# Performance work log

Hardware: AMD Instinct MI355X
Metric: run time of the kernel (lower is better)

## Reference

```python
import jax, jax.numpy as jnp
import numpy as np

K = 16  # kNN neighbors (KnnEncoder default)


def _bn(h, g, s):
    # eval-mode BatchNorm with running mean 0 / var 1 folded into affine
    return h * g + s


def setup_inputs() -> dict:
    key = jax.random.key(0)
    cnt = [0]
    def nk():
        cnt[0] += 1
        return jax.random.fold_in(key, cnt[0])
    B, N = 4, 4096
    def W(i, o):
        return jax.random.normal(nk(), (i, o), jnp.float32) / np.float32(i) ** 0.5
    def bias(d):
        return jnp.zeros((d,), jnp.float32)
    def gamma(d):
        return jnp.ones((d,), jnp.float32) + 0.1 * jax.random.normal(nk(), (d,), jnp.float32)
    def beta(d):
        return 0.1 * jax.random.normal(nk(), (d,), jnp.float32)
    inp = dict(
        pos=jax.random.normal(nk(), (B, N, 3), jnp.float32),
        query_point_idx=jax.random.randint(nk(), (B,), 0, N),
        # PointNetConv local MLP: 6 -> 64 -> 128 -> 256 (plain last)
        cw1=W(6, 64), cb1=bias(64), cg1=gamma(64), cs1=beta(64),
        cw2=W(64, 128), cb2=bias(128), cg2=gamma(128), cs2=beta(128),
        cw3=W(128, 256), cb3=bias(256),
        # GlobalSAModule MLP: 259 -> 256 -> 512 -> 1024 (plain last)
        sw1=W(259, 256), sb1=bias(256), sg1=gamma(256), ss1=beta(256),
        sw2=W(256, 512), sb2=bias(512), sg2=gamma(512), ss2=beta(512),
        sw3=W(512, 1024), sb3=bias(1024),
        # EdgeGraspPredictor: 1280 -> 512 -> 256 -> 16
        pw1=W(1280, 512), pb1=bias(512),
        pw2=W(512, 256), pb2=bias(256),
        pw3=W(256, 16), pb3=bias(16),
    )
    return inp


def reference(pos, query_point_idx, cw1, cb1, cg1, cs1, cw2, cb2, cg2, cs2, cw3, cb3,
              sw1, sb1, sg1, ss1, sw2, sb2, sg2, ss2, sw3, sb3,
              pw1, pb1, pw2, pb2, pw3, pb3):
    B, N, _ = pos.shape
    # kNN within each cloud (self included, as torch_geometric knn with x==y)
    d2 = jnp.sum((pos[:, :, None, :] - pos[:, None, :, :]) ** 2, axis=-1)  # [B,N,N]
    _, idx = jax.lax.top_k(-d2, K)  # [B,N,K] targets for each source point n
    nbr = jax.vmap(lambda p, i: p[i])(pos, idx)  # [B,N,K,3] target positions
    # PointNetConv message: cat([x_j = pos_src, pos_src - pos_tgt])
    src = jnp.broadcast_to(pos[:, :, None, :], (B, N, K, 3))
    h = jnp.concatenate([src, src - nbr], axis=-1)  # [B,N,K,6]
    h = jnp.maximum(_bn(h @ cw1 + cb1, cg1, cs1), 0.0)
    h = jnp.maximum(_bn(h @ cw2 + cb2, cg2, cs2), 0.0)
    m = h @ cw3 + cb3  # [B,N,K,256] per-edge messages
    # scatter-max aggregation at target nodes (every node has its self edge)
    tgt = (idx + (jnp.arange(B) * N)[:, None, None]).reshape(-1)
    x = jax.ops.segment_max(m.reshape(-1, m.shape[-1]), tgt, num_segments=B * N)
    x = x.reshape(B, N, -1)  # [B,N,256] per-point features
    # GlobalSAModule: pointwise MLP then global max pool per cloud
    g = jnp.concatenate([x, pos], axis=-1)  # [B,N,259]
    g = jnp.maximum(_bn(g @ sw1 + sb1, sg1, ss1), 0.0)
    g = jnp.maximum(_bn(g @ sw2 + sb2, sg2, ss2), 0.0)
    g = g @ sw3 + sb3  # [B,N,1024]
    scene = jnp.max(g, axis=1)  # [B,1024]
    # gather query point feature, concat with scene feature, predictor MLP
    q = query_point_idx + jnp.arange(B) * N
    point_feat = x.reshape(B * N, -1)[q]  # [B,256]
    ef = jnp.concatenate([point_feat, scene], axis=-1)  # [B,1280]
    h = jnp.maximum(ef @ pw1 + pb1, 0.0)
    h = jnp.maximum(h @ pw2 + pb2, 0.0)
    return h @ pw3 + pb3  # [B,16]
```

## Files before the change

### kernel.cpp

```cpp
#include <hip/hip_runtime.h>

#define BB 4
#define NN 4096
#define KK 16

typedef unsigned short u16;
typedef unsigned int   u32;
typedef unsigned long long u64;

typedef __attribute__((ext_vector_type(8))) short bf16x8;
typedef __attribute__((ext_vector_type(4))) float f32x4;

__device__ __forceinline__ float b2f(u16 x){ return __uint_as_float(((u32)x) << 16); }
__device__ __forceinline__ u16 f2b(float f){
    u32 u = __float_as_uint(f);
    u32 r = (u + 0x7FFFu + ((u >> 16) & 1u)) >> 16;
    return (u16)r;
}
__device__ __forceinline__ u32 fmap(float f){
    u32 u = __float_as_uint(f);
    return (u & 0x80000000u) ? ~u : (u | 0x80000000u);
}
__device__ __forceinline__ float funmap(u32 u){
    u32 v = (u & 0x80000000u) ? (u ^ 0x80000000u) : ~u;
    return __uint_as_float(v);
}

#define N_ARR 27
__device__ const int ASZ[N_ARR] = {
    49152, 384, 64, 64, 64, 8192, 128, 128, 128, 32768, 256,
    66304, 256, 256, 256, 131072, 512, 512, 512, 524288, 1024,
    655360, 512, 131072, 256, 4096, 16 };
__device__ const int AOFF[N_ARR] = {
    0, 49152, 49536, 49600, 49664, 49728, 57920, 58048, 58176, 58304, 91072,
    91328, 157632, 157888, 158144, 158400, 289472, 289984, 290496, 291008, 815296,
    816320, 1471680, 1472192, 1603264, 1603520, 1607616 };

struct Ptrs { const void* p[N_ARR]; };

#define O_POS 0
#define O_CW1 49152
#define O_CB1 49536
#define O_CG1 49600
#define O_CS1 49664
#define O_CB2 57920
#define O_CG2 58048
#define O_CS2 58176
#define O_CB3 91072
#define O_SW1 91328
#define O_SB1 157632
#define O_SG1 157888
#define O_SS1 158144
#define O_SB2 289472
#define O_SG2 289984
#define O_SS2 290496
#define O_SB3 815296
#define O_PW1 816320
#define O_PB1 1471680
#define O_PW2 1472192
#define O_PB2 1603264
#define O_PW3 1603520
#define O_PB3 1607616

__global__ void detect_kernel(const u16* __restrict__ pos_u16, u32* __restrict__ flag){
    __shared__ int cnt;
    if (threadIdx.x == 0) cnt = 0;
    __syncthreads();
    int c = 0;
    #pragma unroll
    for (int s = 0; s < 4; ++s){
        u16 u = pos_u16[2*(threadIdx.x*4 + s)];
        int e = (u >> 7) & 0xFF;
        c += (e >= 0x68 && e <= 0x82) ? 1 : 0;
    }
    atomicAdd(&cnt, c);
    __syncthreads();
    if (threadIdx.x == 0) *flag = (cnt >= 512) ? 1u : 0u;
}

__device__ __forceinline__ void pack_one_src(const void* __restrict__ src, bool isbf,
                                             u16* __restrict__ dst, int tot, int log2n,
                                             int g, int T){
    const int nmask = (1 << log2n) - 1;
    for (int id = g; id < tot; id += T){
        int i = id & 7, lg = (id >> 3) & 3;
        int rest = id >> 5;
        int n = rest & nmask;
        int ks = rest >> log2n;
        int si = (ks*32 + lg*8 + i) << log2n | n;
        dst[id] = isbf ? ((const u16*)src)[si] : f2b(((const float*)src)[si]);
    }
}

__global__ __launch_bounds__(256) void prep_kernel(Ptrs pt, const u32* __restrict__ flagp,
        float* __restrict__ dst, float* __restrict__ psoa,
        u16* __restrict__ wp2, u16* __restrict__ wp3,
        u16* __restrict__ swp1, u16* __restrict__ swp2, u16* __restrict__ swp3){
    const bool isbf = (*flagp != 0);
    const int T = gridDim.x * 256;
    const int g = blockIdx.x * 256 + threadIdx.x;
    #pragma unroll
    for (int a = 0; a < N_ARR; ++a){
        if (a == 5 || a == 9 || a == 15 || a == 19) continue;
        const int sz = ASZ[a], off = AOFF[a];
        if (isbf){
            const u16* s = (const u16*)pt.p[a];
            for (int i = g; i < sz; i += T) dst[off + i] = b2f(s[i]);
        } else {
            const float* s = (const float*)pt.p[a];
            for (int i = g; i < sz; i += T) dst[off + i] = s[i];
        }
    }
    for (int i = g; i < BB*NN; i += T){
        float x, y, z;
        if (isbf){
            const u16* s = (const u16*)pt.p[0];
            x = b2f(s[3*i]); y = b2f(s[3*i+1]); z = b2f(s[3*i+2]);
        } else {
            const float* s = (const float*)pt.p[0];
            x = s[3*i]; y = s[3*i+1]; z = s[3*i+2];
        }
        psoa[i] = x; psoa[BB*NN + i] = y; psoa[2*BB*NN + i] = z;
    }
    pack_one_src(pt.p[5],  isbf, wp2,    8192,  7, g, T);
    pack_one_src(pt.p[9],  isbf, wp3,   32768,  8, g, T);
    pack_one_src(pt.p[11], isbf, swp1,  65536,  8, g, T);
    pack_one_src(pt.p[15], isbf, swp2, 131072,  9, g, T);
    pack_one_src(pt.p[19], isbf, swp3, 524288, 10, g, T);
}

__global__ __launch_bounds__(1024) void sort_kernel(const float* __restrict__ psoa,
        float* __restrict__ xs, float* __restrict__ ys, float* __restrict__ zs,
        int* __restrict__ sidx){
    __shared__ u64 s[NN];
    const int b = blockIdx.x;
    const int tid = threadIdx.x;
    const float* px = psoa + b*NN;
    const float* py = psoa + BB*NN + b*NN;
    const float* pz = psoa + 2*BB*NN + b*NN;
    for (int i = tid; i < NN; i += 1024)
        s[i] = (((u64)fmap(px[i])) << 32) | (u32)i;
    __syncthreads();
    for (int ksz = 2; ksz <= NN; ksz <<= 1){
        for (int jj = ksz >> 1; jj > 0; jj >>= 1){
            for (int t = tid; t < NN/2; t += 1024){
                int i  = ((t & ~(jj-1)) << 1) | (t & (jj-1));
                int ix = i | jj;
                u64 a = s[i], v = s[ix];
                bool up = ((i & ksz) == 0);
                if ((a > v) == up){ s[i] = v; s[ix] = a; }
            }
            __syncthreads();
        }
    }
    for (int r = tid; r < NN; r += 1024){
        u64 kv = s[r];
        int oi = (int)(u32)(kv & 0xFFFFFFFFu);
        xs[b*NN + r] = funmap((u32)(kv >> 32));
        ys[b*NN + r] = py[oi];
        zs[b*NN + r] = pz[oi];
        sidx[b*NN + r] = oi;
    }
}

#define QCAP 192
__device__ __forceinline__ void refine16(u64* __restrict__ buf, int& cnt, float& tau, int lane){
    u64 loc[3];
    #pragma unroll
    for (int q = 0; q < 3; ++q){
        int p = lane + (q << 6);
        loc[q] = (p < cnt) ? buf[p] : ~0ull;
    }
    u64 m = ~0ull;
    #pragma unroll
    for (int r = 0; r < KK; ++r){
        m = loc[0];
        m = loc[1] < m ? loc[1] : m;
        m = loc[2] < m ? loc[2] : m;
        #pragma unroll
        for (int off = 32; off > 0; off >>= 1){
            u64 o = __shfl_xor(m, off);
            m = o < m ? o : m;
        }
        if (lane == r) buf[r] = m;
        #pragma unroll
        for (int q = 0; q < 3; ++q) if (loc[q] == m) loc[q] = ~0ull;
    }
    cnt = KK;
    tau = __uint_as_float((u32)(m >> 32));
}

__global__ __launch_bounds__(512) void knn_kernel(
        const float* __restrict__ xs, const float* __restrict__ ys,
        const float* __restrict__ zs, const int* __restrict__ sidx,
        int* __restrict__ knn_out, u32* __restrict__ deg){
    __shared__ __align__(16) u64 kbuf[16*QCAP];
    const int b  = blockIdx.x >> 8;
    const int r0 = (blockIdx.x & 255) << 4;
    const float* X = xs + b*NN;
    const float* Y = ys + b*NN;
    const float* Z = zs + b*NN;
    const int*   S = sidx + b*NN;
    const int tid = threadIdx.x;
    const int lane = tid & 63;
    const int wv = tid >> 6;
    const int rA = r0 + wv*2, rB = rA + 1;
    const float axq = X[rA], ayq = Y[rA], azq = Z[rA];
    const float bxq = X[rB], byq = Y[rB], bzq = Z[rB];
    u64* bufA = kbuf + (wv*2)*QCAP;
    u64* bufB = bufA + QCAP;

    float tauA = 3.0e38f, tauB = 3.0e38f;
    int cntA = 0, cntB = 0;
    for (int k = 0; k < 128; ++k){
        int j = (lane < 32) ? (rA - 1 - (k << 5) - lane)
                            : (rA + (k << 5) + (lane - 32));
        bool inr = ((u32)j < (u32)NN);
        int ja = inr ? j : rA;
        float cx = X[ja], cy = Y[ja], cz = Z[ja];
        int sorig = S[ja];
        float dxA = axq - cx, dyA = ayq - cy, dzA = azq - cz;
        float d2A = __fadd_rn(__fadd_rn(__fmul_rn(dxA,dxA), __fmul_rn(dyA,dyA)), __fmul_rn(dzA,dzA));
        float dxB = bxq - cx, dyB = byq - cy, dzB = bzq - cz;
        float d2B = __fadd_rn(__fadd_rn(__fmul_rn(dxB,dxB), __fmul_rn(dyB,dyB)), __fmul_rn(dzB,dzB));
        bool pA = inr && (d2A <= tauA);
        u64 balA = __ballot(pA);
        if (balA){
            int nins = __popcll(balA);
            if (cntA + nins > QCAP) refine16(bufA, cntA, tauA, lane);
            if (pA){
                int ofs = __popcll(balA & ((1ull << lane) - 1ull));
                bufA[cntA + ofs] = (((u64)__float_as_uint(d2A)) << 32) | (u32)sorig;
            }
            cntA += nins;
        }
        bool pB = inr && (d2B <= tauB);
        u64 balB = __ballot(pB);
        if (balB){
            int nins = __popcll(balB);
            if (cntB + nins > QCAP) refine16(bufB, cntB, tauB, lane);
            if (pB){
                int ofs = __popcll(balB & ((1ull << lane) - 1ull));
                bufB[cntB + ofs] = (((u64)__float_as_uint(d2B)) << 32) | (u32)sorig;
            }
            cntB += nins;
        }
        int lo = rA - ((k + 1) << 5) - 1;
        int hi = rA + ((k + 1) << 5);
        float xlo = (lo >= 0) ? X[lo] : -3.0e38f;
        float xhi = (hi < NN) ? X[hi] :  3.0e38f;
        float dLa = axq - xlo, dRa = xhi - axq;
        float dLb = bxq - xlo, dRb = xhi - bxq;
        if (dLa*dLa > tauA && dRa*dRa > tauA && dLb*dLb > tauB && dRb*dRb > tauB) break;
    }
    refine16(bufA, cntA, tauA, lane);
    refine16(bufB, cntB, tauB, lane);
    const int origA = S[rA], origB = S[rB];
    if (lane < KK){
        u64 kA = bufA[lane];
        int jA = (int)(u32)(kA & 0xFFFFFFFFu);
        knn_out[((size_t)(b*NN + origA))*KK + lane] = jA;
        atomicAdd(deg + (b << 12) + jA, 1u);
        u64 kB = bufB[lane];
        int jB = (int)(u32)(kB & 0xFFFFFFFFu);
        knn_out[((size_t)(b*NN + origB))*KK + lane] = jB;
        atomicAdd(deg + (b << 12) + jB, 1u);
    }
}

__global__ __launch_bounds__(1024) void scan_kernel(const u32* __restrict__ deg,
                                                    int* __restrict__ rowstart, u32* __restrict__ cursor){
    __shared__ int lsum[1024];
    const int tid = threadIdx.x;
    const int base = tid * 16;
    int loc[16]; int s = 0;
    #pragma unroll
    for (int q = 0; q < 16; ++q){ loc[q] = (int)deg[base+q]; s += loc[q]; }
    lsum[tid] = s;
    __syncthreads();
    int acc = s;
    for (int ofs = 1; ofs < 1024; ofs <<= 1){
        int t = (tid >= ofs) ? lsum[tid-ofs] : 0;
        __syncthreads();
        acc += t; lsum[tid] = acc;
        __syncthreads();
    }
    int excl = acc - s;
    #pragma unroll
    for (int q = 0; q < 16; ++q){
        rowstart[base+q] = excl; cursor[base+q] = (u32)excl; excl += loc[q];
    }
    if (tid == 1023) rowstart[16384] = excl;
}

__global__ __launch_bounds__(256) void fill_kernel(const int* __restrict__ knn,
                                                   u32* __restrict__ cursor, int* __restrict__ csr){
    int e = blockIdx.x*256 + threadIdx.x;
    int b = e >> 16;
    int t = (b << 12) + knn[e];
    u32 pos = atomicAdd(cursor + t, 1u);
    csr[pos] = e;
}

__device__ __forceinline__ bf16x8 ldfrag(const u16* h, int row, int kofs, int rowstride){
    u32 byte = (u32)((row*rowstride + kofs)*2) ^ (u32)((row & 7) << 4);
    return *(const bf16x8*)((const char*)h + byte);
}
__device__ __forceinline__ void st16(u16* h, int row, int col, int rowstride, float v){
    u32 byte = (u32)((row*rowstride + col)*2) ^ (u32)((row & 7) << 4);
    *(u16*)((char*)h + byte) = f2b(v);
}

__global__ __launch_bounds__(256, 2) void edge_kernel(
    const float* __restrict__ conv, const int* __restrict__ knn,
    const int* __restrict__ rowstart, const int* __restrict__ csr,
    const u16* __restrict__ wp2, const u16* __restrict__ wp3,
    u16* __restrict__ xh)
{
    __shared__ float in6[6][64];
    __shared__ int   lts[64];
    __shared__ int   rs_l[17];
    __shared__ float scw1[384];
    __shared__ float sc1[64], sh1[64];
    __shared__ __align__(16) u16 h1s[64*64];
    __shared__ __align__(16) u16 h2s[64*128];
    __shared__ u32 lsx[16*256];

    const float* posf = conv + O_POS;
    const float* cb1 = conv + O_CB1; const float* cg1 = conv + O_CG1; const float* cs1 = conv + O_CS1;

    const int tid = threadIdx.x;
    const int w   = tid >> 6;
    const int l   = tid & 63;
    const int t0  = blockIdx.x << 4;
    const int b   = t0 >> 12;

    if (tid < 64){ float g1 = cg1[tid]; sc1[tid]=g1; sh1[tid]=cb1[tid]*g1 + cs1[tid]; }
    if (tid < 17) rs_l[tid] = rowstart[t0 + tid];
    for (int u = tid; u < 384; u += 256) scw1[u] = conv[O_CW1 + u];
    #pragma unroll
    for (int q = 0; q < 16; ++q) lsx[q*256 + tid] = 0u;

    const int lr = l & 15, lg = l >> 4;
    const int colb2 = w << 5;
    const int colb3 = w << 6;

    float sc2v[2], sh2v[2], bs3v[4];
    #pragma unroll
    for (int nt = 0; nt < 2; ++nt){
        int c = colb2 + nt*16 + lr;
        float g2 = conv[O_CG2 + c];
        sc2v[nt] = g2; sh2v[nt] = conv[O_CB2 + c]*g2 + conv[O_CS2 + c];
    }
    #pragma unroll
    for (int nt = 0; nt < 4; ++nt) bs3v[nt] = conv[O_CB3 + colb3 + nt*16 + lr];

    __syncthreads();
    const int segstart = rs_l[0], segend = rs_l[16];
    const int nchunk = (segend - segstart + 63) >> 6;

    int curl = -1;
    float run[4];
    #pragma unroll
    for (int nt = 0; nt < 4; ++nt) run[nt] = 0.f;

    for (int ch = 0; ch < nchunk; ++ch){
        __syncthreads();
        if (tid < 64){
            int gpos = segstart + (ch << 6) + tid;
            int lt = -1;
            float ax=0,ay=0,az=0,dx=0,dy=0,dz=0;
            if (gpos < segend){
                lt = 0;
                #pragma unroll
                for (int q = 1; q < 16; ++q) lt += (gpos >= rs_l[q]) ? 1 : 0;
                int e = csr[gpos];
                int i = (e >> 4) & (NN - 1);
                int j = knn[e];
                const float* pi = posf + ((size_t)(b*NN + i))*3;
                const float* pj = posf + ((size_t)(b*NN + j))*3;
                ax = pi[0]; ay = pi[1]; az = pi[2];
                dx = ax - pj[0]; dy = ay - pj[1]; dz = az - pj[2];
            }
            lts[tid] = lt;
            in6[0][tid]=ax; in6[1][tid]=ay; in6[2][tid]=az;
            in6[3][tid]=dx; in6[4][tid]=dy; in6[5][tid]=dz;
        }
        __syncthreads();

        {
            const int e = tid & 63, c0g = (tid >> 6) << 4;
            float a0=in6[0][e], a1=in6[1][e], a2=in6[2][e],
                  a3=in6[3][e], a4=in6[4][e], a5=in6[5][e];
            u32 pk[8];
            #pragma unroll
            for (int ci = 0; ci < 16; ++ci){
                int cc = c0g + ci;
                float acc = a0*scw1[cc]     + a1*scw1[64+cc]  + a2*scw1[128+cc]
                          + a3*scw1[192+cc] + a4*scw1[256+cc] + a5*scw1[320+cc];
                float v = fmaxf(acc*sc1[cc] + sh1[cc], 0.f);
                u32 h = (u32)f2b(v);
                if (ci & 1) pk[ci >> 1] |= h << 16; else pk[ci >> 1] = h;
            }
            u32 base = (u32)(e*128 + c0g*2);
            u32 swz  = (u32)((e & 7) << 4);
            *(uint4*)((char*)h1s + (base ^ swz))        = make_uint4(pk[0],pk[1],pk[2],pk[3]);
            *(uint4*)((char*)h1s + ((base + 16) ^ swz)) = make_uint4(pk[4],pk[5],pk[6],pk[7]);
        }
        __syncthreads();

        {
            f32x4 acc2[4][2];
            #pragma unroll
            for (int mt = 0; mt < 4; ++mt)
                #pragma unroll
                for (int nt = 0; nt < 2; ++nt) acc2[mt][nt] = (f32x4){0.f,0.f,0.f,0.f};
            #pragma unroll
            for (int ks = 0; ks < 2; ++ks){
                bf16x8 bf[2];
                #pragma unroll
                for (int nt = 0; nt < 2; ++nt)
                    bf[nt] = *(const bf16x8*)(wp2 + (((ks*128 + colb2 + nt*16 + lr) << 2) + lg)*8);
                #pragma unroll
                for (int mt = 0; mt < 4; ++mt){
                    bf16x8 a = ldfrag(h1s, mt*16 + lr, ks*32 + lg*8, 64);
                    #pragma unroll
                    for (int nt = 0; nt < 2; ++nt)
                        acc2[mt][nt] = __builtin_amdgcn_mfma_f32_16x16x32_bf16(a, bf[nt], acc2[mt][nt], 0, 0, 0);
                }
            }
            #pragma unroll
            for (int mt = 0; mt < 4; ++mt)
                #pragma unroll
                for (int nt = 0; nt < 2; ++nt)
                    #pragma unroll
                    for (int r = 0; r < 4; ++r){
                        int row = mt*16 + lg*4 + r;
                        float v = fmaxf(acc2[mt][nt][r]*sc2v[nt] + sh2v[nt], 0.f);
                        st16(h2s, row, colb2 + nt*16 + lr, 128, v);
                    }
        }
        __syncthreads();

        {
            f32x4 acc3[4][4];
            #pragma unroll
            for (int mt = 0; mt < 4; ++mt)
                #pragma unroll
                for (int nt = 0; nt < 4; ++nt) acc3[mt][nt] = (f32x4){0.f,0.f,0.f,0.f};
            #pragma unroll
            for (int ks = 0; ks < 4; ++ks){
                bf16x8 bf[4];
                #pragma unroll
                for (int nt = 0; nt < 4; ++nt)
                    bf[nt] = *(const bf16x8*)(wp3 + (((ks*256 + colb3 + nt*16 + lr) << 2) + lg)*8);
                #pragma unroll
                for (int mt = 0; mt < 4; ++mt){
                    bf16x8 a = ldfrag(h2s, mt*16 + lr, ks*32 + lg*8, 128);
                    #pragma unroll
                    for (int nt = 0; nt < 4; ++nt)
                        acc3[mt][nt] = __builtin_amdgcn_mfma_f32_16x16x32_bf16(a, bf[nt], acc3[mt][nt], 0, 0, 0);
                }
            }
            #pragma unroll
            for (int mt = 0; mt < 4; ++mt)
                #pragma unroll
                for (int r = 0; r < 4; ++r){
                    int row = mt*16 + lg*4 + r;
                    int lt = lts[row];
                    if (lt != curl){
                        if (curl >= 0){
                            #pragma unroll
                            for (int nt = 0; nt < 4; ++nt)
                                atomicMax(&lsx[curl*256 + colb3 + nt*16 + lr], fmap(run[nt]));
                        }
                        curl = lt;
                        #pragma unroll
                        for (int nt = 0; nt < 4; ++nt) run[nt] = acc3[mt][nt][r] + bs3v[nt];
                    } else {
                        #pragma unroll
                        for (int nt = 0; nt < 4; ++nt) run[nt] = fmaxf(run[nt], acc3[mt][nt][r] + bs3v[nt]);
                    }
                }
        }
    }
    if (curl >= 0){
        #pragma unroll
        for (int nt = 0; nt < 4; ++nt)
            atomicMax(&lsx[curl*256 + colb3 + nt*16 + lr], fmap(run[nt]));
    }
    __syncthreads();
    #pragma unroll
    for (int q = 0; q < 16; ++q)
        xh[((size_t)(t0+q))*256 + tid] = f2b(funmap(lsx[q*256 + tid]));
}

__global__ __launch_bounds__(256, 3) void sa_kernel(
    const float* __restrict__ conv, const u16* __restrict__ xh,
    const u16* __restrict__ swp1, const u16* __restrict__ swp2, const u16* __restrict__ swp3,
    u32* __restrict__ scene_map)
{
    __shared__ __align__(16) u16 h1s[32*256];
    __shared__ __align__(16) u16 h2s[32*512];
    __shared__ float spw[3][256];
    __shared__ float spx[32], spy[32], spz[32];

    const int tid = threadIdx.x;
    const int w   = tid >> 6;
    const int l   = tid & 63;
    const int lr  = l & 15, lg = l >> 4;
    const int b   = blockIdx.x >> 7;
    const int n0  = (blockIdx.x & 127) << 5;
    const u16* xrow = xh + ((size_t)(b*NN + n0))*256;

    if (tid < 96){
        int p = tid & 31, d = tid >> 5;
        float v = conv[O_POS + ((size_t)(b*NN + n0 + p))*3 + d];
        if (d == 0) spx[p] = v; else if (d == 1) spy[p] = v; else spz[p] = v;
    }
    for (int u = tid; u < 768; u += 256)
        spw[u >> 8][u & 255] = conv[O_SW1 + (256 + (u >> 8))*256 + (u & 255)];
    __syncthreads();

    {
        const int c0 = w << 6;
        float sc1v[4], sh1v[4];
        #pragma unroll
        for (int nt = 0; nt < 4; ++nt){
            int cc = c0 + nt*16 + lr;
            float g = conv[O_SG1 + cc];
            sc1v[nt] = g; sh1v[nt] = conv[O_SB1 + cc]*g + conv[O_SS1 + cc];
        }
        f32x4 acc[2][4];
        #pragma unroll
        for (int mt = 0; mt < 2; ++mt)
            #pragma unroll
            for (int nt = 0; nt < 4; ++nt)
                #pragma unroll
                for (int r = 0; r < 4; ++r){
                    int row = mt*16 + lg*4 + r;
                    int cc  = c0 + nt*16 + lr;
                    acc[mt][nt][r] = spx[row]*spw[0][cc] + spy[row]*spw[1][cc] + spz[row]*spw[2][cc];
                }
        #pragma unroll
        for (int ks = 0; ks < 8; ++ks){
            bf16x8 bf[4];
            #pragma unroll
            for (int nt = 0; nt < 4; ++nt)
                bf[nt] = *(const bf16x8*)(swp1 + (((ks*256 + c0 + nt*16 + lr) << 2) + lg)*8);
            #pragma unroll
            for (int mt = 0; mt < 2; ++mt){
                bf16x8 a = *(const bf16x8*)(xrow + (mt*16 + lr)*256 + ks*32 + lg*8);
                #pragma unroll
                for (int nt = 0; nt < 4; ++nt)
                    acc[mt][nt] = __builtin_amdgcn_mfma_f32_16x16x32_bf16(a, bf[nt], acc[mt][nt], 0, 0, 0);
            }
        }
        #pragma unroll
        for (int mt = 0; mt < 2; ++mt)
            #pragma unroll
            for (int nt = 0; nt < 4; ++nt)
                #pragma unroll
                for (int r = 0; r < 4; ++r){
                    int row = mt*16 + lg*4 + r;
                    float v = fmaxf(acc[mt][nt][r]*sc1v[nt] + sh1v[nt], 0.f);
                    st16(h1s, row, c0 + nt*16 + lr, 256, v);
                }
    }
    __syncthreads();

    {
        const int c0 = w << 7;
        float sc2v[8], sh2v[8];
        #pragma unroll
        for (int nt = 0; nt < 8; ++nt){
            int cc = c0 + nt*16 + lr;
            float g = conv[O_SG2 + cc];
            sc2v[nt] = g; sh2v[nt] = conv[O_SB2 + cc]*g + conv[O_SS2 + cc];
        }
        f32x4 acc[2][8];
        #pragma unroll
        for (int mt = 0; mt < 2; ++mt)
            #pragma unroll
            for (int nt = 0; nt < 8; ++nt) acc[mt][nt] = (f32x4){0.f,0.f,0.f,0.f};
        #pragma unroll
        for (int ks = 0; ks < 8; ++ks){
            bf16x8 bf[8];
            #pragma unroll
            for (int nt = 0; nt < 8; ++nt)
                bf[nt] = *(const bf16x8*)(swp2 + (((ks*512 + c0 + nt*16 + lr) << 2) + lg)*8);
            #pragma unroll
            for (int mt = 0; mt < 2; ++mt){
                bf16x8 a = ldfrag(h1s, mt*16 + lr, ks*32 + lg*8, 256);
                #pragma unroll
                for (int nt = 0; nt < 8; ++nt)
                    acc[mt][nt] = __builtin_amdgcn_mfma_f32_16x16x32_bf16(a, bf[nt], acc[mt][nt], 0, 0, 0);
            }
        }
        #pragma unroll
        for (int mt = 0; mt < 2; ++mt)
            #pragma unroll
            for (int nt = 0; nt < 8; ++nt)
                #pragma unroll
                for (int r = 0; r < 4; ++r){
                    int row = mt*16 + lg*4 + r;
                    float v = fmaxf(acc[mt][nt][r]*sc2v[nt] + sh2v[nt], 0.f);
                    st16(h2s, row, c0 + nt*16 + lr, 512, v);
                }
    }
    __syncthreads();

    #pragma unroll
    for (int half = 0; half < 2; ++half){
        const int c0 = (half << 9) + (w << 7);
        f32x4 acc[2][8];
        #pragma unroll
        for (int mt = 0; mt < 2; ++mt)
            #pragma unroll
            for (int nt = 0; nt < 8; ++nt) acc[mt][nt] = (f32x4){0.f,0.f,0.f,0.f};
        #pragma unroll
        for (int ks = 0; ks < 16; ++ks){
            bf16x8 bf[8];
            #pragma unroll
            for (int nt = 0; nt < 8; ++nt)
                bf[nt] = *(const bf16x8*)(swp3 + (((ks*1024 + c0 + nt*16 + lr) << 2) + lg)*8);
            #pragma unroll
            for (int mt = 0; mt < 2; ++mt){
                bf16x8 a = ldfrag(h2s, mt*16 + lr, ks*32 + lg*8, 512);
                #pragma unroll
                for (int nt = 0; nt < 8; ++nt)
                    acc[mt][nt] = __builtin_amdgcn_mfma_f32_16x16x32_bf16(a, bf[nt], acc[mt][nt], 0, 0, 0);
            }
        }
        #pragma unroll
        for (int nt = 0; nt < 8; ++nt){
            float v = acc[0][nt][0];
            #pragma unroll
            for (int mt = 0; mt < 2; ++mt)
                #pragma unroll
                for (int r = 0; r < 4; ++r) v = fmaxf(v, acc[mt][nt][r]);
            v = fmaxf(v, __shfl_xor(v, 16));
            v = fmaxf(v, __shfl_xor(v, 32));
            if (lg == 0){
                int cc = c0 + nt*16 + lr;
                atomicMax(scene_map + (b << 10) + cc, fmap(v + conv[O_SB3 + cc]));
            }
        }
    }
}

__global__ __launch_bounds__(128) void head1_kernel(
    const float* __restrict__ conv,
    const u16* __restrict__ xh, const u32* __restrict__ scene_map, const int* __restrict__ qidx,
    float* __restrict__ h1out)
{
    __shared__ float ef[1280];
    __shared__ float psum[4][32];
    const float* pw1 = conv + O_PW1; const float* pb1 = conv + O_PB1;
    const int b  = blockIdx.x >> 4;
    const int c0 = (blockIdx.x & 15) << 5;
    const int tid = threadIdx.x;
    const int q = qidx[b];
    for (int u = tid; u < 1280; u += 128){
        float v;
        if (u < 256) v = b2f(xh[(((size_t)(b*NN + q)) << 8) + u]);
        else         v = funmap(scene_map[(b << 10) + (u - 256)]);
        ef[u] = v;
    }
    __syncthreads();
    const int c = c0 + (tid & 31);
    const int rc = tid >> 5;
    float acc = 0.f;
    for (int r = rc*320; r < rc*320 + 320; ++r) acc += ef[r] * pw1[r*512 + c];
    psum[rc][tid & 31] = acc;
    __syncthreads();
    if (tid < 32){
        float a = psum[0][tid] + psum[1][tid] + psum[2][tid] + psum[3][tid] + pb1[c0 + tid];
        h1out[(b << 9) + c0 + tid] = fmaxf(a, 0.f);
    }
}

__global__ __launch_bounds__(256) void head2_kernel(
    const float* __restrict__ conv, const float* __restrict__ h1in,
    const u32* __restrict__ flagp, void* __restrict__ outv)
{
    __shared__ float h1[4][512];
    __shared__ float h2[4][256];
    const float* pw2 = conv + O_PW2; const float* pb2 = conv + O_PB2;
    const float* pw3 = conv + O_PW3; const float* pb3 = conv + O_PB3;
    const int tid = threadIdx.x;
    for (int u = tid; u < 2048; u += 256) h1[u >> 9][u & 511] = h1in[u];
    __syncthreads();
    for (int o = tid; o < 1024; o += 256){
        int b = o >> 8, c = o & 255;
        float acc = pb2[c];
        for (int r = 0; r < 512; ++r) acc += h1[b][r] * pw2[r*256 + c];
        h2[b][c] = fmaxf(acc, 0.f);
    }
    __syncthreads();
    if (tid < 64){
        int b = tid >> 4, c = tid & 15;
        float acc = pb3[c];
        for (int r = 0; r < 256; ++r) acc += h2[b][r] * pw3[r*16 + c];
        if (*flagp) ((u16*)outv)[tid] = f2b(acc);
        else        ((float*)outv)[tid] = acc;
    }
}

extern "C" void kernel_launch(void* const* d_in, const int* in_sizes, int n_in,
                              void* d_out, int out_size, void* d_ws, size_t ws_size,
                              hipStream_t stream){
    (void)in_sizes; (void)n_in; (void)out_size; (void)ws_size;
    const int* qidx = (const int*)d_in[1];

    char* ws = (char*)d_ws;
    u32*  flag      = (u32*)ws;
    float* conv     = (float*)(ws + 1024);
    u16*  wp2       = (u16*)(ws + 6432768);
    u16*  wp3       = (u16*)(ws + 6449152);
    u16*  swp1      = (u16*)(ws + 6514688);
    u16*  swp2      = (u16*)(ws + 6645760);
    u16*  swp3      = (u16*)(ws + 6907904);
    int*  knn       = (int*)(ws + 7956480);
    u32*  deg       = (u32*)(ws + 9005056);
    u32*  scene_map = (u32*)(ws + 9070592);
    int*  rowstart  = (int*)(ws + 9086976);
    u32*  cursor    = (u32*)(ws + 9152576);
    int*  csr       = (int*)(ws + 9218112);
    u16*  xh        = (u16*)(ws + 10266688);
    float* h1ws     = (float*)(ws + 18655296);
    float* psoa     = (float*)(ws + 18663488);
    float* xs       = (float*)(ws + 18860096);
    float* ys       = (float*)(ws + 18925632);
    float* zs       = (float*)(ws + 18991168);
    int*   sidx     = (int*)(ws + 19056704);

    Ptrs pt;
    pt.p[0] = d_in[0];
    for (int k = 1; k < N_ARR; ++k) pt.p[k] = d_in[k + 1];

    hipMemsetAsync(ws + 9005056, 0, 81920, stream);

    detect_kernel <<<1, 256, 0, stream>>>((const u16*)d_in[0], flag);
    prep_kernel   <<<512, 256, 0, stream>>>(pt, flag, conv, psoa, wp2, wp3, swp1, swp2, swp3);
    sort_kernel   <<<BB, 1024, 0, stream>>>(psoa, xs, ys, zs, sidx);
    knn_kernel <<<1024, 512, 0, stream>>>(xs, ys, zs, sidx, knn, deg);
    scan_kernel<<<1, 1024, 0, stream>>>(deg, rowstart, cursor);
    fill_kernel<<<1024, 256, 0, stream>>>(knn, cursor, csr);
    edge_kernel<<<1024, 256, 0, stream>>>(conv, knn, rowstart, csr, wp2, wp3, xh);
    sa_kernel  <<<512, 256, 0, stream>>>(conv, xh, swp1, swp2, swp3, scene_map);
    head1_kernel<<<64, 128, 0, stream>>>(conv, xh, scene_map, qidx, h1ws);
    head2_kernel<<<1, 256, 0, stream>>>(conv, h1ws, flag, (void*)d_out);
}
```

Measured before the change: 394.2 us.

## Split bitonic sort across two blocks per cloud and trim kNN scan loads

The per-cloud bitonic sort is split in two. A first kernel sorts each 2048-element half in its own block, using directions chosen so the halves form a bitonic sequence, and a second kernel does only the final merge, so eight blocks work where four did before. The kNN loop now loads the original index only when some lane passes the threshold. Its early-exit bound reuses candidate x values by shuffle instead of extra global loads, and it tracks each side separately. The cost is an extra kernel launch and a round trip of the keys through global memory.

Result: faster. 384.1 us (-2.6%).

```diff
diff --git a/kernel.cpp b/kernel.cpp
--- a/kernel.cpp
+++ b/kernel.cpp
@@ -129,36 +129,57 @@
     pack_one_src(pt.p[19], isbf, swp3, 524288, 10, g, T);
 }
 
-__global__ __launch_bounds__(1024) void sort_kernel(const float* __restrict__ psoa,
+__global__ __launch_bounds__(1024) void sort1_kernel(const float* __restrict__ psoa,
+                                                     u64* __restrict__ keys){
+    __shared__ u64 s[2048];
+    const int half = blockIdx.x;
+    const int b    = half >> 1;
+    const int base = (half & 1) << 11;
+    const float* px = psoa + b*NN;
+    const int tid = threadIdx.x;
+    for (int i = tid; i < 2048; i += 1024)
+        s[i] = (((u64)fmap(px[base + i])) << 32) | (u32)(base + i);
+    __syncthreads();
+    for (int ksz = 2; ksz <= 2048; ksz <<= 1){
+        for (int jj = ksz >> 1; jj > 0; jj >>= 1){
+            int t = tid;
+            int i  = ((t & ~(jj-1)) << 1) | (t & (jj-1));
+            int ix = i | jj;
+            u64 a = s[i], v = s[ix];
+            bool up = (((base + i) & ksz) == 0);
+            if ((a > v) == up){ s[i] = v; s[ix] = a; }
+            __syncthreads();
+        }
+    }
+    for (int i = tid; i < 2048; i += 1024) keys[b*NN + base + i] = s[i];
+}
+
+__global__ __launch_bounds__(1024) void sort2_kernel(const u64* __restrict__ keys,
+        const float* __restrict__ psoa,
         float* __restrict__ xs, float* __restrict__ ys, float* __restrict__ zs,
         int* __restrict__ sidx){
     __shared__ u64 s[NN];
     const int b = blockIdx.x;
     const int tid = threadIdx.x;
-    const float* px = psoa + b*NN;
-    const float* py = psoa + BB*NN + b*NN;
-    const float* pz = psoa + 2*BB*NN + b*NN;
-    for (int i = tid; i < NN; i += 1024)
-        s[i] = (((u64)fmap(px[i])) << 32) | (u32)i;
-    __syncthreads();
-    for (int ksz = 2; ksz <= NN; ksz <<= 1){
-        for (int jj = ksz >> 1; jj > 0; jj >>= 1){
-            for (int t = tid; t < NN/2; t += 1024){
-                int i  = ((t & ~(jj-1)) << 1) | (t & (jj-1));
-                int ix = i | jj;
-                u64 a = s[i], v = s[ix];
-                bool up = ((i & ksz) == 0);
-                if ((a > v) == up){ s[i] = v; s[ix] = a; }
-            }
-            __syncthreads();
-        }
-    }
+    for (int i = tid; i < NN; i += 1024) s[i] = keys[b*NN + i];
+    __syncthreads();
+    for (int jj = NN >> 1; jj > 0; jj >>= 1){
+        for (int t = tid; t < NN/2; t += 1024){
+            int i  = ((t & ~(jj-1)) << 1) | (t & (jj-1));
+            int ix = i | jj;
+            u64 a = s[i], v = s[ix];
+            if (a > v){ s[i] = v; s[ix] = a; }
+        }
+        __syncthreads();
+    }
+    const float* py = psoa + BB*NN;
+    const float* pz = psoa + 2*BB*NN;
     for (int r = tid; r < NN; r += 1024){
         u64 kv = s[r];
         int oi = (int)(u32)(kv & 0xFFFFFFFFu);
         xs[b*NN + r] = funmap((u32)(kv >> 32));
-        ys[b*NN + r] = py[oi];
-        zs[b*NN + r] = pz[oi];
+        ys[b*NN + r] = py[b*NN + oi];
+        zs[b*NN + r] = pz[b*NN + oi];
         sidx[b*NN + r] = oi;
     }
 }
@@ -218,13 +239,16 @@
         bool inr = ((u32)j < (u32)NN);
         int ja = inr ? j : rA;
         float cx = X[ja], cy = Y[ja], cz = Z[ja];
-        int sorig = S[ja];
         float dxA = axq - cx, dyA = ayq - cy, dzA = azq - cz;
         float d2A = __fadd_rn(__fadd_rn(__fmul_rn(dxA,dxA), __fmul_rn(dyA,dyA)), __fmul_rn(dzA,dzA));
         float dxB = bxq - cx, dyB = byq - cy, dzB = bzq - cz;
         float d2B = __fadd_rn(__fadd_rn(__fmul_rn(dxB,dxB), __fmul_rn(dyB,dyB)), __fmul_rn(dzB,dzB));
         bool pA = inr && (d2A <= tauA);
+        bool pB = inr && (d2B <= tauB);
         u64 balA = __ballot(pA);
+        u64 balB = __ballot(pB);
+        int sorig = 0;
+        if (balA | balB) sorig = S[ja];
         if (balA){
             int nins = __popcll(balA);
             if (cntA + nins > QCAP) refine16(bufA, cntA, tauA, lane);
@@ -234,8 +258,6 @@
             }
             cntA += nins;
         }
-        bool pB = inr && (d2B <= tauB);
-        u64 balB = __ballot(pB);
         if (balB){
             int nins = __popcll(balB);
             if (cntB + nins > QCAP) refine16(bufB, cntB, tauB, lane);
@@ -245,13 +267,15 @@
             }
             cntB += nins;
         }
-        int lo = rA - ((k + 1) << 5) - 1;
-        int hi = rA + ((k + 1) << 5);
-        float xlo = (lo >= 0) ? X[lo] : -3.0e38f;
-        float xhi = (hi < NN) ? X[hi] :  3.0e38f;
-        float dLa = axq - xlo, dRa = xhi - axq;
-        float dLb = bxq - xlo, dRb = xhi - bxq;
-        if (dLa*dLa > tauA && dRa*dRa > tauA && dLb*dLb > tauB && dRb*dRb > tauB) break;
+        float xL = __shfl(cx, 31);
+        float xR = __shfl(cx, 63);
+        bool lex = (rA - ((k + 1) << 5) - 1) < 0;
+        bool rex = (rA + ((k + 1) << 5)) >= NN;
+        float dLa = axq - xL, dRa = xR - axq;
+        float dLb = bxq - xL, dRb = xR - bxq;
+        bool ldone = lex || (dLa*dLa > tauA && dLb*dLb > tauB);
+        bool rdone = rex || (dRa*dRa > tauA && dRb*dRb > tauB);
+        if (ldone && rdone) break;
     }
     refine16(bufA, cntA, tauA, lane);
     refine16(bufB, cntB, tauB, lane);
@@ -734,6 +758,7 @@
     float* ys       = (float*)(ws + 18925632);
     float* zs       = (float*)(ws + 18991168);
     int*   sidx     = (int*)(ws + 19056704);
+    u64*   keys     = (u64*)(ws + 19122240);
 
     Ptrs pt;
     pt.p[0] = d_in[0];
@@ -743,7 +768,8 @@
 
     detect_kernel <<<1, 256, 0, stream>>>((const u16*)d_in[0], flag);
     prep_kernel   <<<512, 256, 0, stream>>>(pt, flag, conv, psoa, wp2, wp3, swp1, swp2, swp3);
-    sort_kernel   <<<BB, 1024, 0, stream>>>(psoa, xs, ys, zs, sidx);
+    sort1_kernel  <<<BB*2, 1024, 0, stream>>>(psoa, keys);
+    sort2_kernel  <<<BB, 1024, 0, stream>>>(keys, psoa, xs, ys, zs, sidx);
     knn_kernel <<<1024, 512, 0, stream>>>(xs, ys, zs, sidx, knn, deg);
     scan_kernel<<<1, 1024, 0, stream>>>(deg, rowstart, cursor);
     fill_kernel<<<1024, 256, 0, stream>>>(knn, cursor, csr);
```
